# Optimization experiments

Hardware: AMD Instinct MI355X
Metric: run time of the kernel (lower is better)

Reference implementation:

```python
import jax, jax.numpy as jnp
import numpy as np

B, N, D, DEG = 16, 8192, 384, 16
K, H, STEPS = 8, 128, 3


def setup_inputs() -> dict:
    key = jax.random.key(0)
    ks = jax.random.split(key, 8)
    s_in = 1.0 / np.sqrt(2 * D)
    s_h = 1.0 / np.sqrt(H)
    return {
        "q_embs": jax.random.normal(ks[0], (B, D), jnp.float32),
        "emb": jax.random.normal(ks[1], (B, N, D), jnp.float32),
        "neighbors": jax.random.randint(ks[2], (B, N, DEG), 0, N, jnp.int32),
        "labels": jax.random.randint(ks[3], (B, N), 0, 2, jnp.int32),
        "W1": jax.random.normal(ks[4], (2 * D, H), jnp.float32) * s_in,
        "b1": jnp.zeros((H,), jnp.float32),
        "W2": jax.random.normal(ks[5], (H, K), jnp.float32) * s_h,
        "b2": jnp.zeros((K,), jnp.float32),
        "P1": jax.random.normal(ks[6], (2 * D, H), jnp.float32) * s_in,
        "pb1": jnp.zeros((H,), jnp.float32),
        "P2": jax.random.normal(ks[7], (H, 1), jnp.float32) * s_h,
        "pb2": jnp.zeros((1,), jnp.float32),
    }


def reference(q_embs, emb, neighbors, labels, W1, b1, W2, b2, P1, pb1, P2, pb2):
    b, n, d = emb.shape
    k = W2.shape[1]
    # inp = [emb | q broadcast]  -> [B, N, 2D]
    inp = jnp.concatenate([emb, jnp.broadcast_to(q_embs[:, None, :], emb.shape)], axis=-1)
    # path_net: sigmoid(MLP) -> [B, N], then +1 at support (label==1) nodes
    path = jax.nn.sigmoid(jax.nn.relu(inp @ P1 + pb1) @ P2 + pb2)[..., 0]
    path = path + labels.astype(path.dtype)
    # coin_net amplitudes scaled by (1 + path)
    amps = (jax.nn.relu(inp @ W1 + b1) @ W2 + b2) * (1.0 + path)[..., None]  # [B,N,K]
    # initial uniform state
    state = jnp.full((b, n, k), 1.0 / np.sqrt(n * k), dtype=emb.dtype)

    # sparse adjacency diffusion: out[i] = sum_{j in nbrs[i]} st[j]
    spmm = jax.vmap(lambda st, nb: st[nb].sum(axis=1))  # st [N,K], nb [N,DEG]

    for _ in range(STEPS):
        st = spmm(state * amps, neighbors)                 # [B,N,K]
        norm = jnp.linalg.norm(st.reshape(b, -1), axis=1)[:, None, None]
        state = jnp.where(norm > 0, st / norm, st)
    return jnp.abs(state).sum(axis=-1)  # [B,N]
```

## Files before the change

kernel.cpp:

```cpp
#include <hip/hip_runtime.h>
#include <cstdint>
#include <cstddef>

#define BB 16
#define NN 8192
#define DD 384
#define HH 128
#define KK 8
#define DEG 16

typedef short bf8_t __attribute__((ext_vector_type(8)));
typedef float f4_t __attribute__((ext_vector_type(4)));

__device__ __forceinline__ unsigned short f2bf(float f) {
  unsigned int u = __float_as_uint(f);
  u += 0x7FFFu + ((u >> 16) & 1u);
  return (unsigned short)(u >> 16);
}

__device__ __forceinline__ bf8_t pack8(float4 f0, float4 f1) {
  union { unsigned short us[8]; bf8_t v; } pk;
  pk.us[0] = f2bf(f0.x); pk.us[1] = f2bf(f0.y);
  pk.us[2] = f2bf(f0.z); pk.us[3] = f2bf(f0.w);
  pk.us[4] = f2bf(f1.x); pk.us[5] = f2bf(f1.y);
  pk.us[6] = f2bf(f1.z); pk.us[7] = f2bf(f1.w);
  return pk.v;
}

__global__ __launch_bounds__(256) void kprep(
    const float* __restrict__ q, const float* __restrict__ W1,
    const float* __restrict__ b1, const float* __restrict__ P1,
    const float* __restrict__ pb1,
    unsigned short* __restrict__ W1t, unsigned short* __restrict__ P1t,
    float* __restrict__ base1, float* __restrict__ baseP,
    float* __restrict__ normsq)
{
  int blk = blockIdx.x, t = threadIdx.x;
  if (blk < 32) {
    int b = blk >> 1, net = blk & 1;
    const float* W = (net ? P1 : W1) + (size_t)DD * HH;
    const float* qb = q + b * DD;
    int h = t & 127, half = t >> 7;
    int d0 = half * 192;
    float a0 = 0.f, a1 = 0.f, a2 = 0.f, a3 = 0.f;
    for (int d = d0; d < d0 + 192; d += 4) {
      a0 = fmaf(qb[d],     W[(size_t)d * HH + h],       a0);
      a1 = fmaf(qb[d + 1], W[(size_t)(d + 1) * HH + h], a1);
      a2 = fmaf(qb[d + 2], W[(size_t)(d + 2) * HH + h], a2);
      a3 = fmaf(qb[d + 3], W[(size_t)(d + 3) * HH + h], a3);
    }
    __shared__ float red[256];
    red[t] = (a0 + a1) + (a2 + a3);
    __syncthreads();
    if (t < 128) {
      float tot = red[t] + red[t + 128] + (net ? pb1[h] : b1[h]);
      (net ? baseP : base1)[b * HH + h] = tot;
    }
  } else {
    int e = (blk - 32) * 3072 + t;
    for (int it = 0; it < 12; ++it, e += 256) {
      int net = e / 49152;
      int r = e - net * 49152;
      int d = r >> 7;
      int h = r & 127;
      float v = (net ? P1 : W1)[d * HH + h];
      (net ? P1t : W1t)[h * DD + d] = f2bf(v);
    }
    if (blk == 32 && t < BB) normsq[t] = 0.f;
  }
}

__global__ __launch_bounds__(512, 6) void kgemm(
    const float* __restrict__ emb,
    const unsigned short* __restrict__ W1t, const unsigned short* __restrict__ P1t,
    const float* __restrict__ base1, const float* __restrict__ baseP,
    const float* __restrict__ W2, const float* __restrict__ P2,
    float* __restrict__ rawp0, float* __restrict__ rawp1,
    float* __restrict__ pslp0, float* __restrict__ pslp1)
{
  __shared__ __align__(16) unsigned short sB[64 * 384];
  __shared__ float sW2a[64 * 9];
  __shared__ float sBase[64];
  __shared__ float sP2[64];

  const int g = blockIdx.x;
  const int job = g >> 9;
  const int net = job >> 1, hh = job & 1;
  const int rowblk = g & 511;
  const int b = rowblk >> 5;
  const int rowbase = (rowblk & 31) * 256;

  const int t = threadIdx.x;
  const int w = t >> 6, lane = t & 63, q = lane >> 4, ln = lane & 15;

  const unsigned short* Wt = (net ? P1t : W1t) + (size_t)hh * 64 * DD;
  {
    int hl = t >> 3, pb = (t & 7) * 6;
#pragma unroll
    for (int i = 0; i < 6; ++i) {
      int p = pb + i;
      uint4 v = *(const uint4*)(Wt + hl * DD + p * 8);
      *(uint4*)((char*)sB + hl * 768 + ((p ^ (hl & 7)) << 4)) = v;
    }
  }
  if (t < 64) sBase[t] = (net ? baseP : base1)[b * HH + hh * 64 + t];
  if (net == 0) {
    if (t < 512) {
      int hl = t >> 3, kk = t & 7;
      sW2a[hl * 9 + kk] = W2[(hh * 64 + hl) * KK + kk];
    }
  } else if (t >= 64 && t < 128) {
    sP2[t - 64] = P2[hh * 64 + (t - 64)];
  }

  const float* ar0 = emb + (size_t)(b * NN + rowbase + w * 32 + ln) * DD + q * 8;
  const float* ar1 = ar0 + (size_t)16 * DD;
  float4 pf0 = ((const float4*)ar0)[0], pf1 = ((const float4*)ar0)[1];
  float4 pf2 = ((const float4*)ar1)[0], pf3 = ((const float4*)ar1)[1];

  f4_t acc[2][4];
  f4_t zero = {0.f, 0.f, 0.f, 0.f};
#pragma unroll
  for (int i = 0; i < 4; ++i) { acc[0][i] = zero; acc[1][i] = zero; }

  __syncthreads();

#pragma unroll
  for (int j = 0; j < 12; ++j) {
    bf8_t af0 = pack8(pf0, pf1);
    bf8_t af1 = pack8(pf2, pf3);
    if (j < 11) {
      const float* p0 = ar0 + (j + 1) * 32;
      const float* p1 = ar1 + (j + 1) * 32;
      pf0 = ((const float4*)p0)[0]; pf1 = ((const float4*)p0)[1];
      pf2 = ((const float4*)p1)[0]; pf3 = ((const float4*)p1)[1];
    }
    const int jb = j * 4;
#pragma unroll
    for (int ct = 0; ct < 4; ++ct) {
      const int hl = ct * 16 + ln;
      bf8_t bf = *(const bf8_t*)((const char*)sB + hl * 768 + (((jb + q) ^ (ln & 7)) << 4));
      acc[0][ct] = __builtin_amdgcn_mfma_f32_16x16x32_bf16(af0, bf, acc[0][ct], 0, 0, 0);
      acc[1][ct] = __builtin_amdgcn_mfma_f32_16x16x32_bf16(af1, bf, acc[1][ct], 0, 0, 0);
    }
  }

  float* rawp = hh ? rawp1 : rawp0;
  float* pslp = hh ? pslp1 : pslp0;
#pragma unroll
  for (int grp = 0; grp < 2; ++grp) {
#pragma unroll
    for (int r = 0; r < 4; ++r) {
      const int grow = rowbase + w * 32 + grp * 16 + q * 4 + r;
      if (net == 0) {
        float s[8];
#pragma unroll
        for (int kk = 0; kk < 8; ++kk) s[kk] = 0.f;
#pragma unroll
        for (int ct = 0; ct < 4; ++ct) {
          int cl = ct * 16 + ln;
          float h1 = fmaxf(acc[grp][ct][r] + sBase[cl], 0.f);
#pragma unroll
          for (int kk = 0; kk < 8; ++kk) s[kk] = fmaf(h1, sW2a[cl * 9 + kk], s[kk]);
        }
#pragma unroll
        for (int off = 1; off < 16; off <<= 1)
#pragma unroll
          for (int kk = 0; kk < 8; ++kk) s[kk] += __shfl_xor(s[kk], off, 64);
        if (ln == 0) {
          float4* dst = (float4*)(rawp + (size_t)(b * NN + grow) * KK);
          dst[0] = make_float4(s[0], s[1], s[2], s[3]);
          dst[1] = make_float4(s[4], s[5], s[6], s[7]);
        }
      } else {
        float ps = 0.f;
#pragma unroll
        for (int ct = 0; ct < 4; ++ct) {
          int cl = ct * 16 + ln;
          float hp = fmaxf(acc[grp][ct][r] + sBase[cl], 0.f);
          ps = fmaf(hp, sP2[cl], ps);
        }
#pragma unroll
        for (int off = 1; off < 16; off <<= 1) ps += __shfl_xor(ps, off, 64);
        if (ln == 0) pslp[b * NN + grow] = ps;
      }
    }
  }
}

__global__ __launch_bounds__(256) void applyscale(
    const float* __restrict__ raw0, const float* __restrict__ raw1,
    const float* __restrict__ psl0, const float* __restrict__ psl1,
    const float* __restrict__ b2, const float* __restrict__ pb2,
    const int* __restrict__ lab, float* __restrict__ planes)
{
  int node = blockIdx.x * 256 + threadIdx.x;
  float ps = psl0[node] + psl1[node] + pb2[0];
  float sc = 1.f + 1.f / (1.f + __expf(-ps)) + (float)lab[node];
  const float4* r0 = (const float4*)(raw0 + (size_t)node * KK);
  const float4* r1 = (const float4*)(raw1 + (size_t)node * KK);
  float4 a0 = r0[0], a1 = r0[1], c0 = r1[0], c1 = r1[1];
  float v[8];
  v[0] = (a0.x + c0.x + b2[0]) * sc; v[1] = (a0.y + c0.y + b2[1]) * sc;
  v[2] = (a0.z + c0.z + b2[2]) * sc; v[3] = (a0.w + c0.w + b2[3]) * sc;
  v[4] = (a1.x + c1.x + b2[4]) * sc; v[5] = (a1.y + c1.y + b2[5]) * sc;
  v[6] = (a1.z + c1.z + b2[6]) * sc; v[7] = (a1.w + c1.w + b2[7]) * sc;
#pragma unroll
  for (int k = 0; k < 8; ++k) planes[(size_t)k * (BB * NN) + node] = v[k];
}

__global__ __launch_bounds__(1024) void sdiff(
    const int* __restrict__ nbr, float* __restrict__ planes,
    float* __restrict__ normsq)
{
  __shared__ float sS[NN];
  const int g = blockIdx.x;
  const int b = g >> 3, k = g & 7;
  const int t = threadIdx.x;
  float* plane = planes + (size_t)k * (BB * NN) + (size_t)b * NN;
  const int* nbase = nbr + (size_t)b * NN * DEG;

  float m[8];
#pragma unroll
  for (int i = 0; i < 8; ++i) {
    float v = plane[t + i * 1024];
    m[i] = v;
    sS[t + i * 1024] = v;
  }
  __syncthreads();

  float g8[8];
#pragma unroll 1
  for (int r = 0; r < 2; ++r) {
#pragma unroll
    for (int i = 0; i < 8; ++i) {
      int n = t + i * 1024;
      const int4* nbp = (const int4*)(nbase + (size_t)n * DEG);
      int4 q0 = nbp[0], q1 = nbp[1], q2 = nbp[2], q3 = nbp[3];
      float a = sS[q0.x] + sS[q0.y] + sS[q0.z] + sS[q0.w]
              + sS[q1.x] + sS[q1.y] + sS[q1.z] + sS[q1.w]
              + sS[q2.x] + sS[q2.y] + sS[q2.z] + sS[q2.w]
              + sS[q3.x] + sS[q3.y] + sS[q3.z] + sS[q3.w];
      g8[i] = a * m[i];
    }
    __syncthreads();
#pragma unroll
    for (int i = 0; i < 8; ++i) sS[t + i * 1024] = g8[i];
    __syncthreads();
  }

  float ss = 0.f;
#pragma unroll
  for (int i = 0; i < 8; ++i) {
    int n = t + i * 1024;
    const int4* nbp = (const int4*)(nbase + (size_t)n * DEG);
    int4 q0 = nbp[0], q1 = nbp[1], q2 = nbp[2], q3 = nbp[3];
    float a = sS[q0.x] + sS[q0.y] + sS[q0.z] + sS[q0.w]
            + sS[q1.x] + sS[q1.y] + sS[q1.z] + sS[q1.w]
            + sS[q2.x] + sS[q2.y] + sS[q2.z] + sS[q2.w]
            + sS[q3.x] + sS[q3.y] + sS[q3.z] + sS[q3.w];
    plane[n] = a;
    ss += a * a;
  }
#pragma unroll
  for (int o = 1; o < 64; o <<= 1) ss += __shfl_xor(ss, o, 64);
  if ((t & 63) == 0) atomicAdd(&normsq[b], ss);
}

__global__ __launch_bounds__(256) void fout(
    const float* __restrict__ planes, const float* __restrict__ normsq,
    float* __restrict__ out)
{
  int node = blockIdx.x * 256 + threadIdx.x;
  float ns = normsq[node >> 13];
  float inv = ns > 0.f ? rsqrtf(ns) : 1.f;
  float s = 0.f;
#pragma unroll
  for (int k = 0; k < 8; ++k)
    s += fabsf(planes[(size_t)k * (BB * NN) + node]);
  out[node] = s * inv;
}

extern "C" void kernel_launch(void* const* d_in, const int* in_sizes, int n_in,
                              void* d_out, int out_size, void* d_ws, size_t ws_size,
                              hipStream_t stream) {
  const float* q   = (const float*)d_in[0];
  const float* emb = (const float*)d_in[1];
  const int*   nbr = (const int*)d_in[2];
  const int*   lab = (const int*)d_in[3];
  const float* W1  = (const float*)d_in[4];
  const float* b1  = (const float*)d_in[5];
  const float* W2  = (const float*)d_in[6];
  const float* b2  = (const float*)d_in[7];
  const float* P1  = (const float*)d_in[8];
  const float* pb1 = (const float*)d_in[9];
  const float* P2  = (const float*)d_in[10];
  const float* pb2 = (const float*)d_in[11];
  float* out = (float*)d_out;

  const size_t NK = (size_t)BB * NN * KK;
  float* ws     = (float*)d_ws;
  float* rawp0  = ws;
  float* rawp1  = rawp0 + NK;
  float* planes = rawp1 + NK;
  float* pslp0  = planes + NK;
  float* pslp1  = pslp0 + (size_t)BB * NN;
  float* base1  = pslp1 + (size_t)BB * NN;
  float* baseP  = base1 + BB * HH;
  float* normsq = baseP + BB * HH;
  unsigned short* W1t = (unsigned short*)(normsq + 16);
  unsigned short* P1t = W1t + (size_t)HH * DD;

  kprep<<<64, 256, 0, stream>>>(q, W1, b1, P1, pb1, W1t, P1t, base1, baseP, normsq);
  kgemm<<<2048, 512, 0, stream>>>(emb, W1t, P1t, base1, baseP, W2, P2,
                                  rawp0, rawp1, pslp0, pslp1);
  applyscale<<<512, 256, 0, stream>>>(rawp0, rawp1, pslp0, pslp1, b2, pb2, lab, planes);
  sdiff<<<128, 1024, 0, stream>>>(nbr, planes, normsq);
  fout<<<512, 256, 0, stream>>>(planes, normsq, out);
}
```

Measured before the change: 488.9 us.

## Split diffusion into three multi-block gather kernels over paired-K planes

```diff
diff --git a/kernel.cpp b/kernel.cpp
--- a/kernel.cpp
+++ b/kernel.cpp
@@ -84,11 +84,12 @@
   __shared__ float sP2[64];
 
   const int g = blockIdx.x;
-  const int job = g >> 9;
+  const int slot = g & 7;
+  const int job = (g >> 3) & 3;
   const int net = job >> 1, hh = job & 1;
-  const int rowblk = g & 511;
-  const int b = rowblk >> 5;
-  const int rowbase = (rowblk & 31) * 256;
+  const int wid = (g >> 5) * 8 + slot;
+  const int b = wid >> 5;
+  const int rowbase = (wid & 31) * 256;
 
   const int t = threadIdx.x;
   const int w = t >> 6, lane = t & 63, q = lane >> 4, ln = lane & 15;
@@ -200,85 +201,90 @@
   const float4* r0 = (const float4*)(raw0 + (size_t)node * KK);
   const float4* r1 = (const float4*)(raw1 + (size_t)node * KK);
   float4 a0 = r0[0], a1 = r0[1], c0 = r1[0], c1 = r1[1];
-  float v[8];
-  v[0] = (a0.x + c0.x + b2[0]) * sc; v[1] = (a0.y + c0.y + b2[1]) * sc;
-  v[2] = (a0.z + c0.z + b2[2]) * sc; v[3] = (a0.w + c0.w + b2[3]) * sc;
-  v[4] = (a1.x + c1.x + b2[4]) * sc; v[5] = (a1.y + c1.y + b2[5]) * sc;
-  v[6] = (a1.z + c1.z + b2[6]) * sc; v[7] = (a1.w + c1.w + b2[7]) * sc;
-#pragma unroll
-  for (int k = 0; k < 8; ++k) planes[(size_t)k * (BB * NN) + node] = v[k];
-}
-
-__global__ __launch_bounds__(1024) void sdiff(
-    const int* __restrict__ nbr, float* __restrict__ planes,
+  float2* p = (float2*)planes;
+  p[0 * (BB * NN) + node] = make_float2((a0.x + c0.x + b2[0]) * sc,
+                                        (a0.y + c0.y + b2[1]) * sc);
+  p[1 * (BB * NN) + node] = make_float2((a0.z + c0.z + b2[2]) * sc,
+                                        (a0.w + c0.w + b2[3]) * sc);
+  p[2 * (BB * NN) + node] = make_float2((a1.x + c1.x + b2[4]) * sc,
+                                        (a1.y + c1.y + b2[5]) * sc);
+  p[3 * (BB * NN) + node] = make_float2((a1.z + c1.z + b2[6]) * sc,
+                                        (a1.w + c1.w + b2[7]) * sc);
+}
+
+template<bool MUL, bool NRM>
+__global__ __launch_bounds__(256) void sgl(
+    const int* __restrict__ nbr, const float* __restrict__ src,
+    const float* __restrict__ mult, float* __restrict__ out,
     float* __restrict__ normsq)
 {
-  __shared__ float sS[NN];
+  __shared__ float2 sS[NN];
   const int g = blockIdx.x;
-  const int b = g >> 3, k = g & 7;
+  const int kp = g & 3;
+  const int rep = (g >> 2) & 7;
+  const int b = g >> 5;
   const int t = threadIdx.x;
-  float* plane = planes + (size_t)k * (BB * NN) + (size_t)b * NN;
-  const int* nbase = nbr + (size_t)b * NN * DEG;
-
-  float m[8];
-#pragma unroll
-  for (int i = 0; i < 8; ++i) {
-    float v = plane[t + i * 1024];
-    m[i] = v;
-    sS[t + i * 1024] = v;
+
+  const size_t pb = (size_t)kp * (BB * NN) + (size_t)b * NN;
+  {
+    const float4* p4 = (const float4*)((const float2*)src + pb);
+    float4* s4 = (float4*)sS;
+#pragma unroll
+    for (int i = 0; i < 16; ++i) s4[t + i * 256] = p4[t + i * 256];
   }
   __syncthreads();
 
-  float g8[8];
-#pragma unroll 1
-  for (int r = 0; r < 2; ++r) {
-#pragma unroll
-    for (int i = 0; i < 8; ++i) {
-      int n = t + i * 1024;
-      const int4* nbp = (const int4*)(nbase + (size_t)n * DEG);
-      int4 q0 = nbp[0], q1 = nbp[1], q2 = nbp[2], q3 = nbp[3];
-      float a = sS[q0.x] + sS[q0.y] + sS[q0.z] + sS[q0.w]
-              + sS[q1.x] + sS[q1.y] + sS[q1.z] + sS[q1.w]
-              + sS[q2.x] + sS[q2.y] + sS[q2.z] + sS[q2.w]
-              + sS[q3.x] + sS[q3.y] + sS[q3.z] + sS[q3.w];
-      g8[i] = a * m[i];
-    }
-    __syncthreads();
-#pragma unroll
-    for (int i = 0; i < 8; ++i) sS[t + i * 1024] = g8[i];
-    __syncthreads();
-  }
-
-  float ss = 0.f;
-#pragma unroll
-  for (int i = 0; i < 8; ++i) {
-    int n = t + i * 1024;
-    const int4* nbp = (const int4*)(nbase + (size_t)n * DEG);
+  const float2* mplane = (const float2*)mult + pb;
+  float2* oplane = (float2*)out + pb;
+  float ssacc = 0.f;
+#pragma unroll
+  for (int u = 0; u < 4; ++u) {
+    int n = rep * 1024 + u * 256 + t;
+    const int4* nbp = (const int4*)(nbr + ((size_t)b * NN + n) * DEG);
     int4 q0 = nbp[0], q1 = nbp[1], q2 = nbp[2], q3 = nbp[3];
-    float a = sS[q0.x] + sS[q0.y] + sS[q0.z] + sS[q0.w]
-            + sS[q1.x] + sS[q1.y] + sS[q1.z] + sS[q1.w]
-            + sS[q2.x] + sS[q2.y] + sS[q2.z] + sS[q2.w]
-            + sS[q3.x] + sS[q3.y] + sS[q3.z] + sS[q3.w];
-    plane[n] = a;
-    ss += a * a;
-  }
-#pragma unroll
-  for (int o = 1; o < 64; o <<= 1) ss += __shfl_xor(ss, o, 64);
-  if ((t & 63) == 0) atomicAdd(&normsq[b], ss);
+    float ax = 0.f, ay = 0.f;
+    float2 v;
+    v = sS[q0.x]; ax += v.x; ay += v.y;
+    v = sS[q0.y]; ax += v.x; ay += v.y;
+    v = sS[q0.z]; ax += v.x; ay += v.y;
+    v = sS[q0.w]; ax += v.x; ay += v.y;
+    v = sS[q1.x]; ax += v.x; ay += v.y;
+    v = sS[q1.y]; ax += v.x; ay += v.y;
+    v = sS[q1.z]; ax += v.x; ay += v.y;
+    v = sS[q1.w]; ax += v.x; ay += v.y;
+    v = sS[q2.x]; ax += v.x; ay += v.y;
+    v = sS[q2.y]; ax += v.x; ay += v.y;
+    v = sS[q2.z]; ax += v.x; ay += v.y;
+    v = sS[q2.w]; ax += v.x; ay += v.y;
+    v = sS[q3.x]; ax += v.x; ay += v.y;
+    v = sS[q3.y]; ax += v.x; ay += v.y;
+    v = sS[q3.z]; ax += v.x; ay += v.y;
+    v = sS[q3.w]; ax += v.x; ay += v.y;
+    if (MUL) { float2 m = mplane[n]; ax *= m.x; ay *= m.y; }
+    oplane[n] = make_float2(ax, ay);
+    if (NRM) ssacc += ax * ax + ay * ay;
+  }
+  if (NRM) {
+#pragma unroll
+    for (int o = 1; o < 64; o <<= 1) ssacc += __shfl_xor(ssacc, o, 64);
+    if ((t & 63) == 0) atomicAdd(&normsq[b], ssacc);
+  }
 }
 
 __global__ __launch_bounds__(256) void fout(
-    const float* __restrict__ planes, const float* __restrict__ normsq,
+    const float* __restrict__ u, const float* __restrict__ normsq,
     float* __restrict__ out)
 {
   int node = blockIdx.x * 256 + threadIdx.x;
   float ns = normsq[node >> 13];
   float inv = ns > 0.f ? rsqrtf(ns) : 1.f;
-  float s = 0.f;
-#pragma unroll
-  for (int k = 0; k < 8; ++k)
-    s += fabsf(planes[(size_t)k * (BB * NN) + node]);
-  out[node] = s * inv;
+  const float2* p = (const float2*)u;
+  float2 v0 = p[0 * (BB * NN) + node];
+  float2 v1 = p[1 * (BB * NN) + node];
+  float2 v2 = p[2 * (BB * NN) + node];
+  float2 v3 = p[3 * (BB * NN) + node];
+  out[node] = (fabsf(v0.x) + fabsf(v0.y) + fabsf(v1.x) + fabsf(v1.y) +
+               fabsf(v2.x) + fabsf(v2.y) + fabsf(v3.x) + fabsf(v3.y)) * inv;
 }
 
 extern "C" void kernel_launch(void* const* d_in, const int* in_sizes, int n_in,
@@ -315,6 +321,8 @@
   kgemm<<<2048, 512, 0, stream>>>(emb, W1t, P1t, base1, baseP, W2, P2,
                                   rawp0, rawp1, pslp0, pslp1);
   applyscale<<<512, 256, 0, stream>>>(rawp0, rawp1, pslp0, pslp1, b2, pb2, lab, planes);
-  sdiff<<<128, 1024, 0, stream>>>(nbr, planes, normsq);
+  sgl<true,  false><<<512, 256, 0, stream>>>(nbr, planes, planes, rawp0, normsq);
+  sgl<true,  false><<<512, 256, 0, stream>>>(nbr, rawp0, planes, rawp1, normsq);
+  sgl<false, true ><<<512, 256, 0, stream>>>(nbr, rawp1, rawp1, planes, normsq);
   fout<<<512, 256, 0, stream>>>(planes, normsq, out);
 }
```

After: 437.1 us. 1.12x faster.
